# Kernel tuning notes

Hardware: AMD Instinct MI355X
Metric: run time of the kernel (lower is better)

## Reference

```python
import jax, jax.numpy as jnp
import numpy as np

NUM_HEADS = 12


def setup_inputs() -> dict:
    key = jax.random.key(0)
    k1, k2, k3, k4 = jax.random.split(key, 4)
    B, N, C = 8, 1024, 768
    x = jax.random.normal(k1, (B, N, C), dtype=jnp.float32)
    # nn.Linear(dim, 3*dim, bias=False): weight applied as x @ W, shape [C, 3C]
    w_qkv = jax.random.normal(k2, (C, 3 * C), dtype=jnp.float32) * (C ** -0.5)
    # nn.Linear(dim, dim) with bias
    w_proj = jax.random.normal(k3, (C, C), dtype=jnp.float32) * (C ** -0.5)
    b_proj = jax.random.normal(k4, (C,), dtype=jnp.float32) * 0.01
    return {"x": x, "w_qkv": w_qkv, "w_proj": w_proj, "b_proj": b_proj, "H": 32, "W": 32}


def reference(x, w_qkv, w_proj, b_proj, H, W):
    B, N, C = x.shape
    nh = NUM_HEADS
    hd = C // nh
    scale = hd ** -0.5
    qkv = (x @ w_qkv).reshape(B, N, 3, nh, hd)
    q, k, v = jnp.moveaxis(qkv, 2, 0)  # each [B, N, nh, hd]
    attn = jnp.einsum("bnhd,bmhd->bhnm", q, k) * scale  # [B, nh, N, N]
    attn = jax.nn.softmax(attn, axis=-1)
    out = jnp.einsum("bhnm,bmhd->bnhd", attn, v).reshape(B, N, C)
    return out @ w_proj + b_proj
```

## Files before the change

kernel.cpp:

```cpp
#include <hip/hip_runtime.h>

typedef __bf16 bf16x8 __attribute__((ext_vector_type(8)));
typedef float f32x4 __attribute__((ext_vector_type(4)));
typedef float f32x16 __attribute__((ext_vector_type(16)));
typedef unsigned short u16;
typedef unsigned int u32;
typedef u16 u16x4 __attribute__((ext_vector_type(4)));
typedef u32 u32x4 __attribute__((ext_vector_type(4)));

__device__ __forceinline__ u16 f2bf(float f) {
    union { float f; u32 u; } x{f};
    u32 r = x.u + 0x7FFFu + ((x.u >> 16) & 1u);
    return (u16)(r >> 16);
}

__device__ __forceinline__ float ex2(float x) {
#if __has_builtin(__builtin_amdgcn_exp2f)
    return __builtin_amdgcn_exp2f(x);
#else
    return __expf(x * 0.6931471805599453f);
#endif
}

__device__ __forceinline__ u32 pkbf(float a, float b) {
    union { float f; u32 u; } ca{a}, cb{b};
    return ((ca.u + 0x8000u) >> 16) | (((cb.u + 0x8000u) >> 16) << 16);
}

#define GLD16(g, l)                                                            \
    __builtin_amdgcn_global_load_lds(                                          \
        (const __attribute__((address_space(1))) u32*)(g),                     \
        (__attribute__((address_space(3))) u32*)(l), 16, 0, 0)

__global__ void convert_bf16(const float* __restrict__ src, u16* __restrict__ dst, int n4) {
    int i = blockIdx.x * blockDim.x + threadIdx.x;
    if (i < n4) {
        float4 f = *(const float4*)(src + (size_t)i * 4);
        u16x4 u = { f2bf(f.x), f2bf(f.y), f2bf(f.z), f2bf(f.w) };
        *(u16x4*)(dst + (size_t)i * 4) = u;
    }
}

__global__ __launch_bounds__(256) void prep_weights(
    const float* __restrict__ wq, const float* __restrict__ wp,
    u16* __restrict__ WqT, u16* __restrict__ WpT)
{
    __shared__ u16 tile[32][33];
    int id = blockIdx.x;
    const float* src; u16* dst; int R, C, bx, by;
    if (id < 1728) { src = wq; dst = WqT; R = 768; C = 2304; bx = (id % 72) * 32; by = (id / 72) * 32; }
    else { id -= 1728; src = wp; dst = WpT; R = 768; C = 768; bx = (id % 24) * 32; by = (id / 24) * 32; }
    int x = threadIdx.x & 31, y = threadIdx.x >> 5;
    #pragma unroll
    for (int i = 0; i < 32; i += 8)
        tile[y + i][x] = f2bf(src[(size_t)(by + y + i) * C + bx + x]);
    __syncthreads();
    #pragma unroll
    for (int i = 0; i < 32; i += 8)
        dst[(size_t)(bx + y + i) * R + by + x] = tile[x][y + i];
}

template <int K>
__global__ __launch_bounds__(256) void gemm_qkv(
    const u16* __restrict__ A,
    const u16* __restrict__ Wt,
    u16* __restrict__ QKV,
    u16* __restrict__ Vt,
    float qscale)
{
    __shared__ __align__(16) u16 As[128 * 64];
    __shared__ __align__(16) u16 Bs[128 * 64];

    int tid = threadIdx.x;
    int wave = tid >> 6, lane = tid & 63;
    int quad = lane >> 4, l16 = lane & 15;
    int wm = (wave >> 1) * 64, wn = (wave & 1) * 64;
    int bm = blockIdx.y * 128, bn = blockIdx.x * 128;
    bool vsec = (bn >= 1536);

    f32x4 acc[4][4] = {};

    int srow = lane >> 3;
    int scg = ((lane & 7) ^ srow) * 8;
    const u16* Ap = A + (size_t)(bm + wave * 32 + srow) * K + scg;
    const u16* Bp = Wt + (size_t)(bn + wave * 32 + srow) * K + scg;

    int fg0 = (((0 * 4 + quad) ^ (l16 & 7)) * 8);
    int fg1 = (((1 * 4 + quad) ^ (l16 & 7)) * 8);

    for (int k0 = 0; k0 < K; k0 += 64) {
        #pragma unroll
        for (int j = 0; j < 4; j++) {
            GLD16(Ap + k0 + (size_t)j * 8 * K, &As[(wave * 32 + j * 8) * 64]);
            GLD16(Bp + k0 + (size_t)j * 8 * K, &Bs[(wave * 32 + j * 8) * 64]);
        }
        __syncthreads();

        #pragma unroll
        for (int h = 0; h < 2; h++) {
            int fg = h ? fg1 : fg0;
            bf16x8 af[4], bfr[4];
            #pragma unroll
            for (int i = 0; i < 4; i++) {
                af[i]  = *(const bf16x8*)&As[(wm + i * 16 + l16) * 64 + fg];
                bfr[i] = *(const bf16x8*)&Bs[(wn + i * 16 + l16) * 64 + fg];
            }
            if (!vsec) {
                #pragma unroll
                for (int mi = 0; mi < 4; mi++)
                    #pragma unroll
                    for (int ni = 0; ni < 4; ni++)
                        acc[mi][ni] = __builtin_amdgcn_mfma_f32_16x16x32_bf16(af[mi], bfr[ni], acc[mi][ni], 0, 0, 0);
            } else {
                #pragma unroll
                for (int mi = 0; mi < 4; mi++)
                    #pragma unroll
                    for (int ni = 0; ni < 4; ni++)
                        acc[mi][ni] = __builtin_amdgcn_mfma_f32_16x16x32_bf16(bfr[ni], af[mi], acc[mi][ni], 0, 0, 0);
            }
        }
        __syncthreads();
    }

    if (!vsec) {
        #pragma unroll
        for (int mi = 0; mi < 4; mi++) {
            #pragma unroll
            for (int ni = 0; ni < 4; ni++) {
                #pragma unroll
                for (int rg = 0; rg < 4; rg++) {
                    int row = bm + wm + mi * 16 + quad * 4 + rg;
                    int col = bn + wn + ni * 16 + l16;
                    float sc = (col < 768) ? qscale : 1.0f;
                    QKV[(size_t)row * 2304 + col] = f2bf(acc[mi][ni][rg] * sc);
                }
            }
        }
    } else {
        #pragma unroll
        for (int mi = 0; mi < 4; mi++) {
            #pragma unroll
            for (int ni = 0; ni < 4; ni++) {
                #pragma unroll
                for (int rg = 0; rg < 4; rg++) {
                    int d = (bn - 1536) + wn + ni * 16 + quad * 4 + rg;
                    int ng = bm + wm + mi * 16 + l16;
                    int b = ng >> 10, n = ng & 1023, h = d >> 6;
                    Vt[((size_t)(b * 12 + h) * 64 + (d & 63)) * 1024 + n] = f2bf(acc[mi][ni][rg]);
                }
            }
        }
    }
}

template <int K>
__global__ __launch_bounds__(256) void gemm_proj(
    const u16* __restrict__ A,
    const u16* __restrict__ Bt,
    float* __restrict__ Cp,
    const float* __restrict__ bias,
    int M, int N)
{
    __shared__ __align__(16) u16 As[128 * 64];
    __shared__ __align__(16) u16 Bs[128 * 64];

    int tid = threadIdx.x;
    int wave = tid >> 6, lane = tid & 63;
    int quad = lane >> 4, l16 = lane & 15;
    int wm = (wave >> 1) * 64, wn = (wave & 1) * 64;
    int bm = blockIdx.y * 128, bn = blockIdx.x * 128;

    f32x4 acc[4][4] = {};

    int srow = lane >> 3;
    int scg = ((lane & 7) ^ srow) * 8;
    const u16* Ap = A + (size_t)(bm + wave * 32 + srow) * K + scg;
    const u16* Bp = Bt + (size_t)(bn + wave * 32 + srow) * K + scg;

    int fg0 = (((0 * 4 + quad) ^ (l16 & 7)) * 8);
    int fg1 = (((1 * 4 + quad) ^ (l16 & 7)) * 8);

    for (int k0 = 0; k0 < K; k0 += 64) {
        #pragma unroll
        for (int j = 0; j < 4; j++) {
            GLD16(Ap + k0 + (size_t)j * 8 * K, &As[(wave * 32 + j * 8) * 64]);
            GLD16(Bp + k0 + (size_t)j * 8 * K, &Bs[(wave * 32 + j * 8) * 64]);
        }
        __syncthreads();

        #pragma unroll
        for (int h = 0; h < 2; h++) {
            int fg = h ? fg1 : fg0;
            bf16x8 af[4], bfr[4];
            #pragma unroll
            for (int i = 0; i < 4; i++) {
                af[i]  = *(const bf16x8*)&As[(wm + i * 16 + l16) * 64 + fg];
                bfr[i] = *(const bf16x8*)&Bs[(wn + i * 16 + l16) * 64 + fg];
            }
            #pragma unroll
            for (int mi = 0; mi < 4; mi++)
                #pragma unroll
                for (int ni = 0; ni < 4; ni++)
                    acc[mi][ni] = __builtin_amdgcn_mfma_f32_16x16x32_bf16(af[mi], bfr[ni], acc[mi][ni], 0, 0, 0);
        }
        __syncthreads();
    }

    #pragma unroll
    for (int mi = 0; mi < 4; mi++) {
        #pragma unroll
        for (int ni = 0; ni < 4; ni++) {
            #pragma unroll
            for (int rg = 0; rg < 4; rg++) {
                int row = bm + wm + mi * 16 + quad * 4 + rg;
                int col = bn + wn + ni * 16 + l16;
                Cp[(size_t)row * N + col] = acc[mi][ni][rg] + bias[col];
            }
        }
    }
}

__global__ __launch_bounds__(256, 4) void attn_kernel(
    const u16* __restrict__ qkv,
    const u16* __restrict__ Vt,
    u16* __restrict__ ctx)
{
    __shared__ __align__(16) u16 Ks[2][4096];
    __shared__ __align__(16) u16 Vs[2][4096];

    int qt = blockIdx.x;
    int bh = blockIdx.y;
    int b = bh / 12, h = bh % 12;
    int tid = threadIdx.x;
    int wave = tid >> 6, lane = tid & 63;
    int l32 = lane & 31, half = lane >> 5;

    const u16* qbase = qkv + (size_t)(b * 1024 + qt * 128 + wave * 32 + l32) * 2304 + h * 64;
    bf16x8 qa[4];
    #pragma unroll
    for (int ks = 0; ks < 4; ks++)
        qa[ks] = *(const bf16x8*)(qbase + ks * 16 + half * 8);

    int srow = lane >> 3;
    int scol = (lane & 7) ^ srow;
    const u16* kA = qkv + (size_t)(b * 1024 + wave * 16 + srow) * 2304 + 768 + h * 64 + scol * 8;
    const u16* vA = Vt + ((size_t)bh * 64 + wave * 16 + srow) * 1024 + scol * 8;

    bf16x8 ones;
    #pragma unroll
    for (int j = 0; j < 8; j++) ((u16*)&ones)[j] = 0x3F80;

    f32x16 o0 = {}, o1 = {}, lsum = {};

    int fgo[4];
    #pragma unroll
    for (int ks = 0; ks < 4; ks++)
        fgo[ks] = (((ks * 2 + half) ^ (lane & 7)) * 8);

    {
        GLD16(kA,            &Ks[0][(wave * 2 + 0) * 512]);
        GLD16(kA + 8 * 2304, &Ks[0][(wave * 2 + 1) * 512]);
        GLD16(vA,            &Vs[0][(wave * 2 + 0) * 512]);
        GLD16(vA + 8 * 1024, &Vs[0][(wave * 2 + 1) * 512]);
    }

    #pragma unroll 2
    for (int kt = 0; kt < 16; kt++) {
        int buf = kt & 1;
        __syncthreads();

        if (kt < 15) {
            const u16* k0 = kA + (size_t)(kt + 1) * (64 * 2304);
            const u16* v0 = vA + (size_t)(kt + 1) * 64;
            GLD16(k0,            &Ks[buf ^ 1][(wave * 2 + 0) * 512]);
            GLD16(k0 + 8 * 2304, &Ks[buf ^ 1][(wave * 2 + 1) * 512]);
            GLD16(v0,            &Vs[buf ^ 1][(wave * 2 + 0) * 512]);
            GLD16(v0 + 8 * 1024, &Vs[buf ^ 1][(wave * 2 + 1) * 512]);
        }

        f32x16 st0 = {}, st1 = {};
        #pragma unroll
        for (int ks = 0; ks < 4; ks++) {
            bf16x8 kf0 = *(const bf16x8*)&Ks[buf][(l32)      * 64 + fgo[ks]];
            bf16x8 kf1 = *(const bf16x8*)&Ks[buf][(32 + l32) * 64 + fgo[ks]];
            st0 = __builtin_amdgcn_mfma_f32_32x32x16_bf16(kf0, qa[ks], st0, 0, 0, 0);
            st1 = __builtin_amdgcn_mfma_f32_32x32x16_bf16(kf1, qa[ks], st1, 0, 0, 0);
        }

        bf16x8 pf[4];
        #pragma unroll
        for (int t = 0; t < 2; t++) {
            u32 pk[8];
            #pragma unroll
            for (int g = 0; g < 4; g++) {
                float p0 = ex2(t ? st1[4 * g + 0] : st0[4 * g + 0]);
                float p1 = ex2(t ? st1[4 * g + 1] : st0[4 * g + 1]);
                float p2 = ex2(t ? st1[4 * g + 2] : st0[4 * g + 2]);
                float p3 = ex2(t ? st1[4 * g + 3] : st0[4 * g + 3]);
                pk[2 * g + 0] = pkbf(p0, p1);
                pk[2 * g + 1] = pkbf(p2, p3);
            }
            u32 rA0 = __shfl_xor(half ? pk[0] : pk[2], 32);
            u32 rA1 = __shfl_xor(half ? pk[1] : pk[3], 32);
            u32 rB0 = __shfl_xor(half ? pk[4] : pk[6], 32);
            u32 rB1 = __shfl_xor(half ? pk[5] : pk[7], 32);
            u32x4 f0 = { half ? rA0 : pk[0], half ? rA1 : pk[1],
                         half ? pk[2] : rA0, half ? pk[3] : rA1 };
            u32x4 f1 = { half ? rB0 : pk[4], half ? rB1 : pk[5],
                         half ? pk[6] : rB0, half ? pk[7] : rB1 };
            union { u32x4 u; bf16x8 b; } c0{f0}, c1{f1};
            pf[2 * t + 0] = c0.b;
            pf[2 * t + 1] = c1.b;
        }

        #pragma unroll
        for (int ks = 0; ks < 4; ks++) {
            bf16x8 v0f = *(const bf16x8*)&Vs[buf][(l32)      * 64 + fgo[ks]];
            bf16x8 v1f = *(const bf16x8*)&Vs[buf][(32 + l32) * 64 + fgo[ks]];
            lsum = __builtin_amdgcn_mfma_f32_32x32x16_bf16(pf[ks], ones, lsum, 0, 0, 0);
            o0   = __builtin_amdgcn_mfma_f32_32x32x16_bf16(pf[ks], v0f, o0, 0, 0, 0);
            o1   = __builtin_amdgcn_mfma_f32_32x32x16_bf16(pf[ks], v1f, o1, 0, 0, 0);
        }
    }

    #pragma unroll
    for (int reg = 0; reg < 16; reg++) {
        float inv = 1.0f / lsum[reg];
        int row = (reg & 3) + 8 * (reg >> 2) + 4 * half;
        int qrow = qt * 128 + wave * 32 + row;
        size_t base = (size_t)(b * 1024 + qrow) * 768 + h * 64 + l32;
        ctx[base]      = f2bf(o0[reg] * inv);
        ctx[base + 32] = f2bf(o1[reg] * inv);
    }
}

extern "C" void kernel_launch(void* const* d_in, const int* in_sizes, int n_in,
                              void* d_out, int out_size, void* d_ws, size_t ws_size,
                              hipStream_t stream) {
    const float* x      = (const float*)d_in[0];
    const float* w_qkv  = (const float*)d_in[1];
    const float* w_proj = (const float*)d_in[2];
    const float* b_proj = (const float*)d_in[3];
    float* out = (float*)d_out;

    const int BN = 8192;
    const int C = 768, C3 = 2304;
    const float CE = 0.18033688011112042f;

    u16* Xb      = (u16*)d_ws;
    u16* Wqkv_t  = Xb + (size_t)BN * C;
    u16* Wproj_t = Wqkv_t + (size_t)C3 * C;
    u16* QKV     = Wproj_t + (size_t)C * C;
    u16* Vt      = QKV + (size_t)BN * C3;
    u16* Ctx     = Vt + (size_t)96 * 64 * 1024;

    convert_bf16<<<(BN * C / 4 + 255) / 256, 256, 0, stream>>>(x, Xb, BN * C / 4);
    prep_weights<<<2304, 256, 0, stream>>>(w_qkv, w_proj, Wqkv_t, Wproj_t);

    gemm_qkv<768><<<dim3(C3 / 128, BN / 128), 256, 0, stream>>>(
        Xb, Wqkv_t, QKV, Vt, CE);

    attn_kernel<<<dim3(8, 96), 256, 0, stream>>>(QKV, Vt, Ctx);

    gemm_proj<768><<<dim3(C / 128, BN / 128), 256, 0, stream>>>(
        Ctx, Wproj_t, out, b_proj, BN, C);
}
```

Baseline: 194.7 us.

## Rewrite QKV GEMM as 256x256 tile, 8-wave, double-buffered pipelined kernel

Replaces the 128x128 single-buffered QKV GEMM with a 256x256 tile kernel using 8 waves, each computing a 128x64 sub-tile. Global-to-LDS loads for the next K tiles are interleaved with MFMA quads, using double-buffered dynamic LDS, explicit waitcnt, barriers and setprio. Blocks are remapped across XCDs for locality. The aim is to hide load latency and raise operand reuse, at the cost of 128KB of LDS per block, more register pressure, and only 288 blocks.

```diff
diff --git a/kernel.cpp b/kernel.cpp
--- a/kernel.cpp
+++ b/kernel.cpp
@@ -60,93 +60,151 @@
         dst[(size_t)(bx + y + i) * R + by + x] = tile[x][y + i];
 }
 
+#define QUAD(AF, BF, I0)                                                       \
+    if (!vsec) {                                                               \
+        _Pragma("unroll") for (int i = 0; i < 4; i++)                          \
+        _Pragma("unroll") for (int n = 0; n < 4; n++)                          \
+            acc[(I0) + i][n] = __builtin_amdgcn_mfma_f32_16x16x32_bf16(        \
+                AF[(I0) + i], BF[n], acc[(I0) + i][n], 0, 0, 0);               \
+    } else {                                                                   \
+        _Pragma("unroll") for (int i = 0; i < 4; i++)                          \
+        _Pragma("unroll") for (int n = 0; n < 4; n++)                          \
+            acc[(I0) + i][n] = __builtin_amdgcn_mfma_f32_16x16x32_bf16(        \
+                BF[n], AF[(I0) + i], acc[(I0) + i][n], 0, 0, 0);               \
+    }
+
+#define STAGE_A8(tile, hh)                                                     \
+    { const u16* g_ = Ap + (size_t)((hh) * 128) * K + (tile) * 64;             \
+      u16* d_ = ldsA + ((tile) & 1) * 16384 + ((hh) * 128 + wave * 16) * 64;   \
+      GLD16(g_,         d_);                                                   \
+      GLD16(g_ + 8 * K, d_ + 8 * 64); }
+
+#define STAGE_B8(tile, hh)                                                     \
+    { const u16* g_ = Bp + (size_t)((hh) * 128) * K + (tile) * 64;             \
+      u16* d_ = ldsB + ((tile) & 1) * 16384 + ((hh) * 128 + wave * 16) * 64;   \
+      GLD16(g_,         d_);                                                   \
+      GLD16(g_ + 8 * K, d_ + 8 * 64); }
+
 template <int K>
-__global__ __launch_bounds__(256) void gemm_qkv(
+__global__ __launch_bounds__(512, 2) void gemm_qkv8(
     const u16* __restrict__ A,
     const u16* __restrict__ Wt,
     u16* __restrict__ QKV,
     u16* __restrict__ Vt,
     float qscale)
 {
-    __shared__ __align__(16) u16 As[128 * 64];
-    __shared__ __align__(16) u16 Bs[128 * 64];
-
+    extern __shared__ __align__(16) u16 lds[];
+
+    constexpr int NT = K / 64;
     int tid = threadIdx.x;
     int wave = tid >> 6, lane = tid & 63;
     int quad = lane >> 4, l16 = lane & 15;
-    int wm = (wave >> 1) * 64, wn = (wave & 1) * 64;
-    int bm = blockIdx.y * 128, bn = blockIdx.x * 128;
+    int wm = (wave >> 2) * 128, wn = (wave & 3) * 64;
+
+    int id = blockIdx.x;
+    int lin = (id & 7) * 36 + (id >> 3);
+    int bm = (lin / 9) * 256;
+    int bn = (lin % 9) * 256;
     bool vsec = (bn >= 1536);
 
-    f32x4 acc[4][4] = {};
+    f32x4 acc[8][4] = {};
 
     int srow = lane >> 3;
-    int scg = ((lane & 7) ^ srow) * 8;
-    const u16* Ap = A + (size_t)(bm + wave * 32 + srow) * K + scg;
-    const u16* Bp = Wt + (size_t)(bn + wave * 32 + srow) * K + scg;
-
-    int fg0 = (((0 * 4 + quad) ^ (l16 & 7)) * 8);
-    int fg1 = (((1 * 4 + quad) ^ (l16 & 7)) * 8);
-
-    for (int k0 = 0; k0 < K; k0 += 64) {
-        #pragma unroll
-        for (int j = 0; j < 4; j++) {
-            GLD16(Ap + k0 + (size_t)j * 8 * K, &As[(wave * 32 + j * 8) * 64]);
-            GLD16(Bp + k0 + (size_t)j * 8 * K, &Bs[(wave * 32 + j * 8) * 64]);
-        }
-        __syncthreads();
-
-        #pragma unroll
-        for (int h = 0; h < 2; h++) {
-            int fg = h ? fg1 : fg0;
-            bf16x8 af[4], bfr[4];
-            #pragma unroll
-            for (int i = 0; i < 4; i++) {
-                af[i]  = *(const bf16x8*)&As[(wm + i * 16 + l16) * 64 + fg];
-                bfr[i] = *(const bf16x8*)&Bs[(wn + i * 16 + l16) * 64 + fg];
-            }
-            if (!vsec) {
-                #pragma unroll
-                for (int mi = 0; mi < 4; mi++)
-                    #pragma unroll
-                    for (int ni = 0; ni < 4; ni++)
-                        acc[mi][ni] = __builtin_amdgcn_mfma_f32_16x16x32_bf16(af[mi], bfr[ni], acc[mi][ni], 0, 0, 0);
-            } else {
-                #pragma unroll
-                for (int mi = 0; mi < 4; mi++)
-                    #pragma unroll
-                    for (int ni = 0; ni < 4; ni++)
-                        acc[mi][ni] = __builtin_amdgcn_mfma_f32_16x16x32_bf16(bfr[ni], af[mi], acc[mi][ni], 0, 0, 0);
-            }
-        }
-        __syncthreads();
+    int scg = (lane & 7) ^ srow;
+    const u16* Ap = A  + (size_t)(bm + wave * 16 + srow) * K + scg * 8;
+    const u16* Bp = Wt + (size_t)(bn + wave * 16 + srow) * K + scg * 8;
+
+    int fg0 = ((0 * 4 + quad) ^ (l16 & 7)) * 8;
+    int fg1 = ((1 * 4 + quad) ^ (l16 & 7)) * 8;
+
+    u16* ldsA = lds;
+    u16* ldsB = lds + 32768;
+
+    STAGE_A8(0, 0); STAGE_A8(0, 1); STAGE_B8(0, 0); STAGE_B8(0, 1);
+    STAGE_A8(1, 0); STAGE_A8(1, 1);
+    asm volatile("s_waitcnt vmcnt(4)" ::: "memory");
+    __builtin_amdgcn_s_barrier();
+
+    #pragma unroll 2
+    for (int t = 0; t < NT; ++t) {
+        const u16* As = ldsA + (t & 1) * 16384;
+        const u16* Bs = ldsB + (t & 1) * 16384;
+
+        bf16x8 a0[8], a1[8], b0[4], b1[4];
+
+        #pragma unroll
+        for (int n = 0; n < 4; n++)
+            b0[n] = *(const bf16x8*)&Bs[(wn + n * 16 + l16) * 64 + fg0];
+        #pragma unroll
+        for (int i = 0; i < 8; i++)
+            a0[i] = *(const bf16x8*)&As[(wm + i * 16 + l16) * 64 + fg0];
+        if (t + 1 < NT) STAGE_B8(t + 1, 0);
+        __builtin_amdgcn_s_barrier();
+        __builtin_amdgcn_s_setprio(1);
+        QUAD(a0, b0, 0);
+        __builtin_amdgcn_s_setprio(0);
+        __builtin_amdgcn_s_barrier();
+
+        #pragma unroll
+        for (int n = 0; n < 4; n++)
+            b1[n] = *(const bf16x8*)&Bs[(wn + n * 16 + l16) * 64 + fg1];
+        #pragma unroll
+        for (int i = 0; i < 8; i++)
+            a1[i] = *(const bf16x8*)&As[(wm + i * 16 + l16) * 64 + fg1];
+        if (t + 1 < NT) STAGE_B8(t + 1, 1);
+        __builtin_amdgcn_s_barrier();
+        __builtin_amdgcn_s_setprio(1);
+        QUAD(a0, b0, 4);
+        __builtin_amdgcn_s_setprio(0);
+        asm volatile("s_waitcnt lgkmcnt(0)" ::: "memory");
+        __builtin_amdgcn_s_barrier();
+        __builtin_amdgcn_sched_barrier(0);
+
+        if (t + 2 < NT) STAGE_A8(t + 2, 0);
+        __builtin_amdgcn_s_barrier();
+        __builtin_amdgcn_s_setprio(1);
+        QUAD(a1, b1, 0);
+        __builtin_amdgcn_s_setprio(0);
+        __builtin_amdgcn_s_barrier();
+        __builtin_amdgcn_sched_barrier(0);
+
+        if (t + 2 < NT) STAGE_A8(t + 2, 1);
+        __builtin_amdgcn_s_barrier();
+        __builtin_amdgcn_s_setprio(1);
+        QUAD(a1, b1, 4);
+        __builtin_amdgcn_s_setprio(0);
+        if (t + 1 < NT) {
+            if (t + 2 < NT) { asm volatile("s_waitcnt vmcnt(4)" ::: "memory"); }
+            else            { asm volatile("s_waitcnt vmcnt(0)" ::: "memory"); }
+        }
+        __builtin_amdgcn_s_barrier();
     }
 
     if (!vsec) {
-        #pragma unroll
-        for (int mi = 0; mi < 4; mi++) {
-            #pragma unroll
-            for (int ni = 0; ni < 4; ni++) {
+        float sc = (bn < 768) ? qscale : 1.0f;
+        #pragma unroll
+        for (int i = 0; i < 8; i++) {
+            #pragma unroll
+            for (int n = 0; n < 4; n++) {
                 #pragma unroll
                 for (int rg = 0; rg < 4; rg++) {
-                    int row = bm + wm + mi * 16 + quad * 4 + rg;
-                    int col = bn + wn + ni * 16 + l16;
-                    float sc = (col < 768) ? qscale : 1.0f;
-                    QKV[(size_t)row * 2304 + col] = f2bf(acc[mi][ni][rg] * sc);
+                    int row = bm + wm + i * 16 + quad * 4 + rg;
+                    int col = bn + wn + n * 16 + l16;
+                    QKV[(size_t)row * 2304 + col] = f2bf(acc[i][n][rg] * sc);
                 }
             }
         }
     } else {
         #pragma unroll
-        for (int mi = 0; mi < 4; mi++) {
-            #pragma unroll
-            for (int ni = 0; ni < 4; ni++) {
+        for (int i = 0; i < 8; i++) {
+            #pragma unroll
+            for (int n = 0; n < 4; n++) {
                 #pragma unroll
                 for (int rg = 0; rg < 4; rg++) {
-                    int d = (bn - 1536) + wn + ni * 16 + quad * 4 + rg;
-                    int ng = bm + wm + mi * 16 + l16;
-                    int b = ng >> 10, n = ng & 1023, h = d >> 6;
-                    Vt[((size_t)(b * 12 + h) * 64 + (d & 63)) * 1024 + n] = f2bf(acc[mi][ni][rg]);
+                    int d = (bn - 1536) + wn + n * 16 + quad * 4 + rg;
+                    int ng = bm + wm + i * 16 + l16;
+                    int b = ng >> 10, nn = ng & 1023, h = d >> 6;
+                    Vt[((size_t)(b * 12 + h) * 64 + (d & 63)) * 1024 + nn] = f2bf(acc[i][n][rg]);
                 }
             }
         }
@@ -354,11 +412,17 @@
     u16* Vt      = QKV + (size_t)BN * C3;
     u16* Ctx     = Vt + (size_t)96 * 64 * 1024;
 
+    static bool s_attr = false;
+    if (!s_attr) {
+        (void)hipFuncSetAttribute((const void*)gemm_qkv8<768>,
+                                  hipFuncAttributeMaxDynamicSharedMemorySize, 131072);
+        s_attr = true;
+    }
+
     convert_bf16<<<(BN * C / 4 + 255) / 256, 256, 0, stream>>>(x, Xb, BN * C / 4);
     prep_weights<<<2304, 256, 0, stream>>>(w_qkv, w_proj, Wqkv_t, Wproj_t);
 
-    gemm_qkv<768><<<dim3(C3 / 128, BN / 128), 256, 0, stream>>>(
-        Xb, Wqkv_t, QKV, Vt, CE);
+    gemm_qkv8<768><<<288, 512, 131072, stream>>>(Xb, Wqkv_t, QKV, Vt, CE);
 
     attn_kernel<<<dim3(8, 96), 256, 0, stream>>>(QKV, Vt, Ctx);
 
```

After: 364.5 us. 87.2% more time.

## Double-buffer LDS tiles in QKV and projection GEMMs to overlap loads

Applied to the files above, without the earlier changes.

Both GEMM kernels now keep two LDS buffers for the A and B tiles. Each iteration issues the global-to-LDS loads for the next K tile before running the MFMA loop on the current tile, with one barrier per iteration instead of two. This hides global load latency behind compute. In exchange, LDS use per block doubles, which may lower how many blocks fit on each CU.

```diff
diff --git a/kernel.cpp b/kernel.cpp
--- a/kernel.cpp
+++ b/kernel.cpp
@@ -68,8 +68,10 @@
     u16* __restrict__ Vt,
     float qscale)
 {
-    __shared__ __align__(16) u16 As[128 * 64];
-    __shared__ __align__(16) u16 Bs[128 * 64];
+    __shared__ __align__(16) u16 As[2][128 * 64];
+    __shared__ __align__(16) u16 Bs[2][128 * 64];
+
+    constexpr int NT = K / 64;
 
     int tid = threadIdx.x;
     int wave = tid >> 6, lane = tid & 63;
@@ -88,13 +90,23 @@
     int fg0 = (((0 * 4 + quad) ^ (l16 & 7)) * 8);
     int fg1 = (((1 * 4 + quad) ^ (l16 & 7)) * 8);
 
-    for (int k0 = 0; k0 < K; k0 += 64) {
-        #pragma unroll
-        for (int j = 0; j < 4; j++) {
-            GLD16(Ap + k0 + (size_t)j * 8 * K, &As[(wave * 32 + j * 8) * 64]);
-            GLD16(Bp + k0 + (size_t)j * 8 * K, &Bs[(wave * 32 + j * 8) * 64]);
-        }
-        __syncthreads();
+    #pragma unroll
+    for (int j = 0; j < 4; j++) {
+        GLD16(Ap + (size_t)j * 8 * K, &As[0][(wave * 32 + j * 8) * 64]);
+        GLD16(Bp + (size_t)j * 8 * K, &Bs[0][(wave * 32 + j * 8) * 64]);
+    }
+    __syncthreads();
+
+    for (int t = 0; t < NT; ++t) {
+        int buf = t & 1;
+
+        if (t + 1 < NT) {
+            #pragma unroll
+            for (int j = 0; j < 4; j++) {
+                GLD16(Ap + (t + 1) * 64 + (size_t)j * 8 * K, &As[buf ^ 1][(wave * 32 + j * 8) * 64]);
+                GLD16(Bp + (t + 1) * 64 + (size_t)j * 8 * K, &Bs[buf ^ 1][(wave * 32 + j * 8) * 64]);
+            }
+        }
 
         #pragma unroll
         for (int h = 0; h < 2; h++) {
@@ -102,8 +114,8 @@
             bf16x8 af[4], bfr[4];
             #pragma unroll
             for (int i = 0; i < 4; i++) {
-                af[i]  = *(const bf16x8*)&As[(wm + i * 16 + l16) * 64 + fg];
-                bfr[i] = *(const bf16x8*)&Bs[(wn + i * 16 + l16) * 64 + fg];
+                af[i]  = *(const bf16x8*)&As[buf][(wm + i * 16 + l16) * 64 + fg];
+                bfr[i] = *(const bf16x8*)&Bs[buf][(wn + i * 16 + l16) * 64 + fg];
             }
             if (!vsec) {
                 #pragma unroll
@@ -119,6 +131,7 @@
                         acc[mi][ni] = __builtin_amdgcn_mfma_f32_16x16x32_bf16(bfr[ni], af[mi], acc[mi][ni], 0, 0, 0);
             }
         }
+
         __syncthreads();
     }
 
@@ -161,8 +174,10 @@
     const float* __restrict__ bias,
     int M, int N)
 {
-    __shared__ __align__(16) u16 As[128 * 64];
-    __shared__ __align__(16) u16 Bs[128 * 64];
+    __shared__ __align__(16) u16 As[2][128 * 64];
+    __shared__ __align__(16) u16 Bs[2][128 * 64];
+
+    constexpr int NT = K / 64;
 
     int tid = threadIdx.x;
     int wave = tid >> 6, lane = tid & 63;
@@ -180,13 +195,23 @@
     int fg0 = (((0 * 4 + quad) ^ (l16 & 7)) * 8);
     int fg1 = (((1 * 4 + quad) ^ (l16 & 7)) * 8);
 
-    for (int k0 = 0; k0 < K; k0 += 64) {
-        #pragma unroll
-        for (int j = 0; j < 4; j++) {
-            GLD16(Ap + k0 + (size_t)j * 8 * K, &As[(wave * 32 + j * 8) * 64]);
-            GLD16(Bp + k0 + (size_t)j * 8 * K, &Bs[(wave * 32 + j * 8) * 64]);
-        }
-        __syncthreads();
+    #pragma unroll
+    for (int j = 0; j < 4; j++) {
+        GLD16(Ap + (size_t)j * 8 * K, &As[0][(wave * 32 + j * 8) * 64]);
+        GLD16(Bp + (size_t)j * 8 * K, &Bs[0][(wave * 32 + j * 8) * 64]);
+    }
+    __syncthreads();
+
+    for (int t = 0; t < NT; ++t) {
+        int buf = t & 1;
+
+        if (t + 1 < NT) {
+            #pragma unroll
+            for (int j = 0; j < 4; j++) {
+                GLD16(Ap + (t + 1) * 64 + (size_t)j * 8 * K, &As[buf ^ 1][(wave * 32 + j * 8) * 64]);
+                GLD16(Bp + (t + 1) * 64 + (size_t)j * 8 * K, &Bs[buf ^ 1][(wave * 32 + j * 8) * 64]);
+            }
+        }
 
         #pragma unroll
         for (int h = 0; h < 2; h++) {
@@ -194,8 +219,8 @@
             bf16x8 af[4], bfr[4];
             #pragma unroll
             for (int i = 0; i < 4; i++) {
-                af[i]  = *(const bf16x8*)&As[(wm + i * 16 + l16) * 64 + fg];
-                bfr[i] = *(const bf16x8*)&Bs[(wn + i * 16 + l16) * 64 + fg];
+                af[i]  = *(const bf16x8*)&As[buf][(wm + i * 16 + l16) * 64 + fg];
+                bfr[i] = *(const bf16x8*)&Bs[buf][(wn + i * 16 + l16) * 64 + fg];
             }
             #pragma unroll
             for (int mi = 0; mi < 4; mi++)
@@ -203,6 +228,7 @@
                 for (int ni = 0; ni < 4; ni++)
                     acc[mi][ni] = __builtin_amdgcn_mfma_f32_16x16x32_bf16(af[mi], bfr[ni], acc[mi][ni], 0, 0, 0);
         }
+
         __syncthreads();
     }
 
```

New measurement: 205.6 us. 1.06x slower.

## Triple-buffer QKV GEMM with 8 waves, prefetch pipeline and XCD-aware block swizzle

Applied to the files above, without the earlier changes.

Rewrites the QKV projection GEMM to use 512 threads (8 waves, each owning a 32x64 sub-tile) and a 3-stage LDS ring buffer in dynamic shared memory, issuing global-to-LDS loads two k-tiles ahead and splitting the A and B prefetch across the two half-steps. It adds s_setprio around MFMA bursts and interleaved barriers, and remaps the 1-D grid so consecutive blocks on each XCD share row tiles. The aim is to hide global load latency behind MFMA work that was previously serialized by load-then-sync, at the cost of 96KB of LDS per block and more barriers.

```diff
diff --git a/kernel.cpp b/kernel.cpp
--- a/kernel.cpp
+++ b/kernel.cpp
@@ -60,85 +60,127 @@
         dst[(size_t)(bx + y + i) * R + by + x] = tile[x][y + i];
 }
 
+#define MM8(A0_, A1_, B0_, B1_, B2_, B3_)                                       \
+    if (!vsec) {                                                                \
+        acc[0][0] = __builtin_amdgcn_mfma_f32_16x16x32_bf16(A0_, B0_, acc[0][0], 0, 0, 0); \
+        acc[0][1] = __builtin_amdgcn_mfma_f32_16x16x32_bf16(A0_, B1_, acc[0][1], 0, 0, 0); \
+        acc[0][2] = __builtin_amdgcn_mfma_f32_16x16x32_bf16(A0_, B2_, acc[0][2], 0, 0, 0); \
+        acc[0][3] = __builtin_amdgcn_mfma_f32_16x16x32_bf16(A0_, B3_, acc[0][3], 0, 0, 0); \
+        acc[1][0] = __builtin_amdgcn_mfma_f32_16x16x32_bf16(A1_, B0_, acc[1][0], 0, 0, 0); \
+        acc[1][1] = __builtin_amdgcn_mfma_f32_16x16x32_bf16(A1_, B1_, acc[1][1], 0, 0, 0); \
+        acc[1][2] = __builtin_amdgcn_mfma_f32_16x16x32_bf16(A1_, B2_, acc[1][2], 0, 0, 0); \
+        acc[1][3] = __builtin_amdgcn_mfma_f32_16x16x32_bf16(A1_, B3_, acc[1][3], 0, 0, 0); \
+    } else {                                                                    \
+        acc[0][0] = __builtin_amdgcn_mfma_f32_16x16x32_bf16(B0_, A0_, acc[0][0], 0, 0, 0); \
+        acc[0][1] = __builtin_amdgcn_mfma_f32_16x16x32_bf16(B1_, A0_, acc[0][1], 0, 0, 0); \
+        acc[0][2] = __builtin_amdgcn_mfma_f32_16x16x32_bf16(B2_, A0_, acc[0][2], 0, 0, 0); \
+        acc[0][3] = __builtin_amdgcn_mfma_f32_16x16x32_bf16(B3_, A0_, acc[0][3], 0, 0, 0); \
+        acc[1][0] = __builtin_amdgcn_mfma_f32_16x16x32_bf16(B0_, A1_, acc[1][0], 0, 0, 0); \
+        acc[1][1] = __builtin_amdgcn_mfma_f32_16x16x32_bf16(B1_, A1_, acc[1][1], 0, 0, 0); \
+        acc[1][2] = __builtin_amdgcn_mfma_f32_16x16x32_bf16(B2_, A1_, acc[1][2], 0, 0, 0); \
+        acc[1][3] = __builtin_amdgcn_mfma_f32_16x16x32_bf16(B3_, A1_, acc[1][3], 0, 0, 0); \
+    }
+
+#define STG_A(t, j) GLD16(Ap + (t) * 64 + (size_t)(j) * 8 * K,                  \
+                          &Asb[((t) % 3) * 8192 + (wave * 16 + (j) * 8) * 64])
+#define STG_B(t, j) GLD16(Bp + (t) * 64 + (size_t)(j) * 8 * K,                  \
+                          &Bsb[((t) % 3) * 8192 + (wave * 16 + (j) * 8) * 64])
+
 template <int K>
-__global__ __launch_bounds__(256) void gemm_qkv(
+__global__ __launch_bounds__(512, 2) void gemm_qkv(
     const u16* __restrict__ A,
     const u16* __restrict__ Wt,
     u16* __restrict__ QKV,
     u16* __restrict__ Vt,
     float qscale)
 {
-    __shared__ __align__(16) u16 As[128 * 64];
-    __shared__ __align__(16) u16 Bs[128 * 64];
+    extern __shared__ __align__(16) u16 lds[];
+    u16* Asb = lds;
+    u16* Bsb = lds + 3 * 8192;
+
+    constexpr int NT = K / 64;
 
     int tid = threadIdx.x;
     int wave = tid >> 6, lane = tid & 63;
     int quad = lane >> 4, l16 = lane & 15;
-    int wm = (wave >> 1) * 64, wn = (wave & 1) * 64;
-    int bm = blockIdx.y * 128, bn = blockIdx.x * 128;
+    int wm = (wave >> 1) * 32, wn = (wave & 1) * 64;
+
+    int id = blockIdx.x;
+    int lin = (id & 7) * 144 + (id >> 3);
+    int bm = (lin / 18) * 128;
+    int bn = (lin % 18) * 128;
     bool vsec = (bn >= 1536);
 
-    f32x4 acc[4][4] = {};
+    f32x4 acc[2][4] = {};
 
     int srow = lane >> 3;
     int scg = ((lane & 7) ^ srow) * 8;
-    const u16* Ap = A + (size_t)(bm + wave * 32 + srow) * K + scg;
-    const u16* Bp = Wt + (size_t)(bn + wave * 32 + srow) * K + scg;
-
-    int fg0 = (((0 * 4 + quad) ^ (l16 & 7)) * 8);
-    int fg1 = (((1 * 4 + quad) ^ (l16 & 7)) * 8);
-
-    for (int k0 = 0; k0 < K; k0 += 64) {
-        #pragma unroll
-        for (int j = 0; j < 4; j++) {
-            GLD16(Ap + k0 + (size_t)j * 8 * K, &As[(wave * 32 + j * 8) * 64]);
-            GLD16(Bp + k0 + (size_t)j * 8 * K, &Bs[(wave * 32 + j * 8) * 64]);
-        }
-        __syncthreads();
-
-        #pragma unroll
-        for (int h = 0; h < 2; h++) {
-            int fg = h ? fg1 : fg0;
-            bf16x8 af[4], bfr[4];
-            #pragma unroll
-            for (int i = 0; i < 4; i++) {
-                af[i]  = *(const bf16x8*)&As[(wm + i * 16 + l16) * 64 + fg];
-                bfr[i] = *(const bf16x8*)&Bs[(wn + i * 16 + l16) * 64 + fg];
-            }
-            if (!vsec) {
-                #pragma unroll
-                for (int mi = 0; mi < 4; mi++)
-                    #pragma unroll
-                    for (int ni = 0; ni < 4; ni++)
-                        acc[mi][ni] = __builtin_amdgcn_mfma_f32_16x16x32_bf16(af[mi], bfr[ni], acc[mi][ni], 0, 0, 0);
-            } else {
-                #pragma unroll
-                for (int mi = 0; mi < 4; mi++)
-                    #pragma unroll
-                    for (int ni = 0; ni < 4; ni++)
-                        acc[mi][ni] = __builtin_amdgcn_mfma_f32_16x16x32_bf16(bfr[ni], af[mi], acc[mi][ni], 0, 0, 0);
-            }
-        }
-        __syncthreads();
+    const u16* Ap = A  + (size_t)(bm + wave * 16 + srow) * K + scg;
+    const u16* Bp = Wt + (size_t)(bn + wave * 16 + srow) * K + scg;
+
+    int fg0 = ((0 * 4 + quad) ^ (l16 & 7)) * 8;
+    int fg1 = ((1 * 4 + quad) ^ (l16 & 7)) * 8;
+
+    STG_A(0, 0); STG_A(0, 1); STG_B(0, 0); STG_B(0, 1);
+    STG_A(1, 0); STG_A(1, 1); STG_B(1, 0); STG_B(1, 1);
+    asm volatile("s_waitcnt vmcnt(4)" ::: "memory");
+    __builtin_amdgcn_s_barrier();
+
+    #pragma unroll
+    for (int t = 0; t < NT; ++t) {
+        const u16* Ab = &Asb[(t % 3) * 8192];
+        const u16* Bb = &Bsb[(t % 3) * 8192];
+
+        {
+            bf16x8 a0 = *(const bf16x8*)&Ab[(wm +  0 + l16) * 64 + fg0];
+            bf16x8 a1 = *(const bf16x8*)&Ab[(wm + 16 + l16) * 64 + fg0];
+            bf16x8 b0 = *(const bf16x8*)&Bb[(wn +  0 + l16) * 64 + fg0];
+            bf16x8 b1 = *(const bf16x8*)&Bb[(wn + 16 + l16) * 64 + fg0];
+            bf16x8 b2 = *(const bf16x8*)&Bb[(wn + 32 + l16) * 64 + fg0];
+            bf16x8 b3 = *(const bf16x8*)&Bb[(wn + 48 + l16) * 64 + fg0];
+            if (t + 2 < NT) { STG_A(t + 2, 0); STG_A(t + 2, 1); }
+            __builtin_amdgcn_s_barrier();
+            __builtin_amdgcn_s_setprio(1);
+            MM8(a0, a1, b0, b1, b2, b3);
+            __builtin_amdgcn_s_setprio(0);
+            __builtin_amdgcn_s_barrier();
+        }
+
+        {
+            bf16x8 a0 = *(const bf16x8*)&Ab[(wm +  0 + l16) * 64 + fg1];
+            bf16x8 a1 = *(const bf16x8*)&Ab[(wm + 16 + l16) * 64 + fg1];
+            bf16x8 b0 = *(const bf16x8*)&Bb[(wn +  0 + l16) * 64 + fg1];
+            bf16x8 b1 = *(const bf16x8*)&Bb[(wn + 16 + l16) * 64 + fg1];
+            bf16x8 b2 = *(const bf16x8*)&Bb[(wn + 32 + l16) * 64 + fg1];
+            bf16x8 b3 = *(const bf16x8*)&Bb[(wn + 48 + l16) * 64 + fg1];
+            if (t + 2 < NT) { STG_B(t + 2, 0); STG_B(t + 2, 1); }
+            __builtin_amdgcn_s_barrier();
+            __builtin_amdgcn_s_setprio(1);
+            MM8(a0, a1, b0, b1, b2, b3);
+            __builtin_amdgcn_s_setprio(0);
+            if (t + 2 < NT)      { asm volatile("s_waitcnt vmcnt(4)" ::: "memory"); }
+            else if (t + 1 < NT) { asm volatile("s_waitcnt vmcnt(0)" ::: "memory"); }
+            __builtin_amdgcn_s_barrier();
+        }
     }
 
     if (!vsec) {
-        #pragma unroll
-        for (int mi = 0; mi < 4; mi++) {
+        float sc = (bn < 768) ? qscale : 1.0f;
+        #pragma unroll
+        for (int mi = 0; mi < 2; mi++) {
             #pragma unroll
             for (int ni = 0; ni < 4; ni++) {
                 #pragma unroll
                 for (int rg = 0; rg < 4; rg++) {
                     int row = bm + wm + mi * 16 + quad * 4 + rg;
                     int col = bn + wn + ni * 16 + l16;
-                    float sc = (col < 768) ? qscale : 1.0f;
                     QKV[(size_t)row * 2304 + col] = f2bf(acc[mi][ni][rg] * sc);
                 }
             }
         }
     } else {
         #pragma unroll
-        for (int mi = 0; mi < 4; mi++) {
+        for (int mi = 0; mi < 2; mi++) {
             #pragma unroll
             for (int ni = 0; ni < 4; ni++) {
                 #pragma unroll
@@ -152,6 +194,10 @@
         }
     }
 }
+
+#undef MM8
+#undef STG_A
+#undef STG_B
 
 template <int K>
 __global__ __launch_bounds__(256) void gemm_proj(
@@ -354,11 +400,17 @@
     u16* Vt      = QKV + (size_t)BN * C3;
     u16* Ctx     = Vt + (size_t)96 * 64 * 1024;
 
+    static bool s_attr = false;
+    if (!s_attr) {
+        (void)hipFuncSetAttribute((const void*)gemm_qkv<768>,
+                                  hipFuncAttributeMaxDynamicSharedMemorySize, 98304);
+        s_attr = true;
+    }
+
     convert_bf16<<<(BN * C / 4 + 255) / 256, 256, 0, stream>>>(x, Xb, BN * C / 4);
     prep_weights<<<2304, 256, 0, stream>>>(w_qkv, w_proj, Wqkv_t, Wproj_t);
 
-    gemm_qkv<768><<<dim3(C3 / 128, BN / 128), 256, 0, stream>>>(
-        Xb, Wqkv_t, QKV, Vt, CE);
+    gemm_qkv<768><<<1152, 512, 98304, stream>>>(Xb, Wqkv_t, QKV, Vt, CE);
 
     attn_kernel<<<dim3(8, 96), 256, 0, stream>>>(QKV, Vt, Ctx);
 
```

Measured after the change: 193.6 us. No clear change (-0.6%).
